# Kernel tuning notes

Measured on AMD Instinct MI355X. Metric: run time of the kernel, lower is better.

## Reference

```python
import jax, jax.numpy as jnp
import numpy as np

N_NODES = 100000
N_EDGES = 3200000
IN_DIM = 64
N_SEQ = 8
HID1 = 256
HID2 = 128
END = 64
OUT = 1


def _glorot(key, shape):
    fan_in, fan_out = shape
    lim = (6.0 / (fan_in + fan_out)) ** 0.5
    return jax.random.uniform(key, shape, jnp.float32, -lim, lim)


def setup_inputs() -> dict:
    key = jax.random.key(0)
    ks = jax.random.split(key, 10)
    features = jax.random.normal(ks[0], (N_NODES, IN_DIM, N_SEQ), jnp.float32)
    src = jax.random.randint(ks[1], (N_EDGES,), 0, N_NODES, jnp.int32)
    dst = jax.random.randint(ks[2], (N_EDGES,), 0, N_NODES, jnp.int32)
    return {
        "features": features,
        "src": src,
        "dst": dst,
        "W1": _glorot(ks[3], (IN_DIM * N_SEQ, HID1)),
        "b1": jnp.zeros((HID1,), jnp.float32),
        "W2": _glorot(ks[4], (HID1, HID2)),
        "b2": jnp.zeros((HID2,), jnp.float32),
        "Wo1": _glorot(ks[5], (HID2, END)),
        "bo1": jnp.zeros((END,), jnp.float32),
        "Wo2": _glorot(ks[6], (END, OUT)),
        "bo2": jnp.zeros((OUT,), jnp.float32),
    }


def _graph_conv(x, src, dst, W, b):
    # DGL GraphConv, norm='both': D_out^{-1/2} pre-scale, sum-aggregate, D_in^{-1/2} post-scale.
    n = x.shape[0]
    ones = jnp.ones((src.shape[0],), x.dtype)
    deg_out = jnp.clip(jax.ops.segment_sum(ones, src, num_segments=n), 1.0)
    deg_in = jnp.clip(jax.ops.segment_sum(ones, dst, num_segments=n), 1.0)
    x = x * jax.lax.rsqrt(deg_out)[:, None]
    # mult-first vs aggregate-first is mathematically identical; project to smaller dim first
    if W.shape[0] > W.shape[1]:
        x = x @ W
        agg = jax.ops.segment_sum(x[src], dst, num_segments=n)
    else:
        agg = jax.ops.segment_sum(x[src], dst, num_segments=n) @ W
    return agg * jax.lax.rsqrt(deg_in)[:, None] + b


def reference(features, src, dst, W1, b1, W2, b2, Wo1, bo1, Wo2, bo2):
    x = features.reshape(features.shape[0], IN_DIM * N_SEQ)  # [N, in_dim*n_seq]
    x = jax.nn.relu(_graph_conv(x, src, dst, W1, b1))
    x = _graph_conv(x, src, dst, W2, b2)
    x = jax.nn.relu(x @ Wo1 + bo1)
    return x @ Wo2 + bo2
```

## Files before the change

### kernel.cpp

```cpp
#include <hip/hip_runtime.h>
#include <hip/hip_bf16.h>
#include <hip/hip_fp16.h>

#define N_NODES 100000
#define N_EDGES 3200000
#define DIM0 512
#define DIM1 256
#define DIM2 128
#define DIM3 64
#define NSB 98

typedef _Float16 f16x8 __attribute__((ext_vector_type(8)));
typedef float f32x4 __attribute__((ext_vector_type(4)));


__global__ __launch_bounds__(256) void k_hist(const int* __restrict__ src,
                                              const int* __restrict__ dst,
                                              int* __restrict__ cnt_out,
                                              int* __restrict__ cnt_in,
                                              int* __restrict__ pos) {
    int e = blockIdx.x * 256 + threadIdx.x;
    if (e < N_EDGES) {
        atomicAdd(&cnt_out[src[e]], 1);
        pos[e] = atomicAdd(&cnt_in[dst[e]], 1);
    }
}

__global__ __launch_bounds__(1024) void k_scan_a(const int* __restrict__ cnt,
                                                 int* __restrict__ excl,
                                                 int* __restrict__ bsum) {
    __shared__ int buf[1024];
    int tid = threadIdx.x;
    int i = blockIdx.x * 1024 + tid;
    int v = (i < N_NODES) ? cnt[i] : 0;
    buf[tid] = v;
    __syncthreads();
    #pragma unroll
    for (int off = 1; off < 1024; off <<= 1) {
        int t = (tid >= off) ? buf[tid - off] : 0;
        __syncthreads();
        buf[tid] += t;
        __syncthreads();
    }
    if (i < N_NODES) excl[i] = buf[tid] - v;
    if (tid == 1023) bsum[blockIdx.x] = buf[1023];
}

__global__ __launch_bounds__(128) void k_scan_b(const int* __restrict__ bsum,
                                                int* __restrict__ boff) {
    __shared__ int buf[128];
    int tid = threadIdx.x;
    int v = (tid < NSB) ? bsum[tid] : 0;
    buf[tid] = v;
    __syncthreads();
    #pragma unroll
    for (int off = 1; off < 128; off <<= 1) {
        int t = (tid >= off) ? buf[tid - off] : 0;
        __syncthreads();
        buf[tid] += t;
        __syncthreads();
    }
    if (tid < NSB) boff[tid] = buf[tid] - v;
    if (tid == 127) boff[NSB] = buf[127];
}

__global__ __launch_bounds__(256) void k_scan_c(const int* __restrict__ excl,
                                                const int* __restrict__ boff,
                                                int* __restrict__ row_ptr) {
    int i = blockIdx.x * 256 + threadIdx.x;
    if (i < N_NODES) row_ptr[i] = excl[i] + boff[i >> 10];
    if (i == 0) row_ptr[N_NODES] = boff[NSB];
}

__global__ __launch_bounds__(256) void k_scatter(const int* __restrict__ src,
                                                 const int* __restrict__ dst,
                                                 const int* __restrict__ row_ptr,
                                                 const int* __restrict__ pos,
                                                 int* __restrict__ esrc) {
    int e = blockIdx.x * 256 + threadIdx.x;
    if (e < N_EDGES) esrc[row_ptr[dst[e]] + pos[e]] = src[e];
}

__global__ __launch_bounds__(256) void k_scales(const int* __restrict__ cnt_out,
                                                const int* __restrict__ cnt_in,
                                                float* __restrict__ s_out,
                                                float* __restrict__ s_in) {
    int i = blockIdx.x * 256 + threadIdx.x;
    if (i < N_NODES) {
        int co = cnt_out[i]; if (co < 1) co = 1;
        int ci = cnt_in[i];  if (ci < 1) ci = 1;
        s_out[i] = rsqrtf((float)co);
        s_in[i]  = rsqrtf((float)ci);
    }
}


__global__ __launch_bounds__(256) void k_cvtW1(const float* __restrict__ W1,
                                               __half* __restrict__ W1t) {
    int idx = blockIdx.x * 256 + threadIdx.x;
    if (idx < DIM0 * DIM1) {
        int k = idx / DIM1, n = idx % DIM1;
        W1t[n * DIM0 + k] = __float2half(W1[idx]);
    }
}

__global__ __launch_bounds__(256) void k_cvtW2(const float* __restrict__ W2,
                                               __half* __restrict__ W2t) {
    int idx = blockIdx.x * 256 + threadIdx.x;
    if (idx < DIM1 * DIM2) {
        int k = idx / DIM2, n = idx % DIM2;
        W2t[n * DIM1 + k] = __float2half(W2[idx]);
    }
}


__global__ __launch_bounds__(256) void k_gemm1(const float* __restrict__ feat,
                                               const float* __restrict__ s_out,
                                               const __half* __restrict__ W1t,
                                               __half* __restrict__ y) {
    __shared__ __align__(16) _Float16 As[64][40];
    __shared__ __align__(16) _Float16 Bs[256][40];
    int tid = threadIdx.x;
    int wv = tid >> 6, lane = tid & 63;
    int m16 = lane & 15, quad = lane >> 4;
    int n0 = blockIdx.x * 64;

    int srow = tid >> 2;
    int scol = (tid & 3) * 8;
    int gr = n0 + srow;
    bool avalid = gr < N_NODES;
    int grc = avalid ? gr : (N_NODES - 1);
    float ascale = avalid ? s_out[gr] : 0.0f;
    const float* aptr = feat + (size_t)grc * DIM0 + scol;
    int bn = tid >> 2;
    int bc = (tid & 3) * 8;

    f32x4 acc[4][4] = {};
    for (int k0 = 0; k0 < DIM0; k0 += 32) {
        float4 f0 = *(const float4*)(aptr + k0);
        float4 f1 = *(const float4*)(aptr + k0 + 4);
        __syncthreads();
        {
            f16x8 h;
            h[0] = (_Float16)(f0.x * ascale); h[1] = (_Float16)(f0.y * ascale);
            h[2] = (_Float16)(f0.z * ascale); h[3] = (_Float16)(f0.w * ascale);
            h[4] = (_Float16)(f1.x * ascale); h[5] = (_Float16)(f1.y * ascale);
            h[6] = (_Float16)(f1.z * ascale); h[7] = (_Float16)(f1.w * ascale);
            *(f16x8*)&As[srow][scol] = h;
        }
        #pragma unroll
        for (int p = 0; p < 4; ++p) {
            int n = p * 64 + bn;
            f16x8 v = *(const f16x8*)(W1t + (size_t)n * DIM0 + k0 + bc);
            *(f16x8*)&Bs[n][bc] = v;
        }
        __syncthreads();
        f16x8 af[4], bf[4];
        #pragma unroll
        for (int r = 0; r < 4; ++r) af[r] = *(const f16x8*)&As[r * 16 + m16][quad * 8];
        #pragma unroll
        for (int c = 0; c < 4; ++c) bf[c] = *(const f16x8*)&Bs[wv * 64 + c * 16 + m16][quad * 8];
        #pragma unroll
        for (int r = 0; r < 4; ++r)
            #pragma unroll
            for (int c = 0; c < 4; ++c)
                acc[r][c] = __builtin_amdgcn_mfma_f32_16x16x32_f16(af[r], bf[c], acc[r][c], 0, 0, 0);
    }
    #pragma unroll
    for (int r = 0; r < 4; ++r) {
        #pragma unroll
        for (int i = 0; i < 4; ++i) {
            int row = n0 + r * 16 + quad * 4 + i;
            if (row < N_NODES) {
                #pragma unroll
                for (int c = 0; c < 4; ++c) {
                    int col = wv * 64 + c * 16 + m16;
                    y[(size_t)row * DIM1 + col] = __float2half(acc[r][c][i]);
                }
            }
        }
    }
}


__global__ __launch_bounds__(256) void k_agg256(const int* __restrict__ row_ptr,
                                                const int* __restrict__ esrc,
                                                const __half* __restrict__ y1,
                                                const float* __restrict__ s_in,
                                                const float* __restrict__ s_out,
                                                const float* __restrict__ b1,
                                                __half* __restrict__ x2) {
    int wave = threadIdx.x >> 6;
    int lane = threadIdx.x & 63;
    int n = blockIdx.x * 4 + wave;
    int beg = row_ptr[n], end = row_ptr[n + 1];
    const uint2* ybase = (const uint2*)y1;
    float4 acc = make_float4(0.f, 0.f, 0.f, 0.f);
    int i = beg;
    for (; i + 4 <= end; i += 4) {
        int s0 = esrc[i], s1 = esrc[i + 1], s2 = esrc[i + 2], s3 = esrc[i + 3];
        uint2 r0 = ybase[(size_t)s0 * 64 + lane];
        uint2 r1 = ybase[(size_t)s1 * 64 + lane];
        uint2 r2 = ybase[(size_t)s2 * 64 + lane];
        uint2 r3 = ybase[(size_t)s3 * 64 + lane];
        float2 a0 = __half22float2(*(__half2*)&r0.x), b0 = __half22float2(*(__half2*)&r0.y);
        float2 a1 = __half22float2(*(__half2*)&r1.x), b1v = __half22float2(*(__half2*)&r1.y);
        float2 a2 = __half22float2(*(__half2*)&r2.x), b2v = __half22float2(*(__half2*)&r2.y);
        float2 a3 = __half22float2(*(__half2*)&r3.x), b3v = __half22float2(*(__half2*)&r3.y);
        acc.x += a0.x + a1.x + a2.x + a3.x;
        acc.y += a0.y + a1.y + a2.y + a3.y;
        acc.z += b0.x + b1v.x + b2v.x + b3v.x;
        acc.w += b0.y + b1v.y + b2v.y + b3v.y;
    }
    for (; i < end; ++i) {
        uint2 r = ybase[(size_t)esrc[i] * 64 + lane];
        float2 a = __half22float2(*(__half2*)&r.x), b = __half22float2(*(__half2*)&r.y);
        acc.x += a.x; acc.y += a.y; acc.z += b.x; acc.w += b.y;
    }
    float si = s_in[n];
    float so = s_out[n];
    float4 bb = *(const float4*)&b1[lane * 4];
    acc.x = fmaxf(acc.x * si + bb.x, 0.f) * so;
    acc.y = fmaxf(acc.y * si + bb.y, 0.f) * so;
    acc.z = fmaxf(acc.z * si + bb.z, 0.f) * so;
    acc.w = fmaxf(acc.w * si + bb.w, 0.f) * so;
    union { uint2 u; __half2 h[2]; } cv;
    cv.h[0] = __floats2half2_rn(acc.x, acc.y);
    cv.h[1] = __floats2half2_rn(acc.z, acc.w);
    *(uint2*)&x2[(size_t)n * DIM1 + lane * 4] = cv.u;
}


__global__ __launch_bounds__(256) void k_gemm2(const __half* __restrict__ x2,
                                               const __half* __restrict__ W2t,
                                               __half* __restrict__ y) {
    __shared__ __align__(16) _Float16 As[64][40];
    __shared__ __align__(16) _Float16 Bs[128][40];
    int tid = threadIdx.x;
    int wv = tid >> 6, lane = tid & 63;
    int m16 = lane & 15, quad = lane >> 4;
    int n0 = blockIdx.x * 64;

    int srow = tid >> 2;
    int scol = (tid & 3) * 8;
    int gr = n0 + srow;
    int grc = (gr < N_NODES) ? gr : (N_NODES - 1);
    const __half* aptr = x2 + (size_t)grc * DIM1 + scol;
    int bn = tid >> 2;
    int bc = (tid & 3) * 8;

    f32x4 acc[4][2] = {};
    for (int k0 = 0; k0 < DIM1; k0 += 32) {
        f16x8 av = *(const f16x8*)(aptr + k0);
        __syncthreads();
        *(f16x8*)&As[srow][scol] = av;
        #pragma unroll
        for (int p = 0; p < 2; ++p) {
            int n = p * 64 + bn;
            f16x8 v = *(const f16x8*)(W2t + (size_t)n * DIM1 + k0 + bc);
            *(f16x8*)&Bs[n][bc] = v;
        }
        __syncthreads();
        f16x8 af[4], bf[2];
        #pragma unroll
        for (int r = 0; r < 4; ++r) af[r] = *(const f16x8*)&As[r * 16 + m16][quad * 8];
        #pragma unroll
        for (int c = 0; c < 2; ++c) bf[c] = *(const f16x8*)&Bs[wv * 32 + c * 16 + m16][quad * 8];
        #pragma unroll
        for (int r = 0; r < 4; ++r)
            #pragma unroll
            for (int c = 0; c < 2; ++c)
                acc[r][c] = __builtin_amdgcn_mfma_f32_16x16x32_f16(af[r], bf[c], acc[r][c], 0, 0, 0);
    }
    #pragma unroll
    for (int r = 0; r < 4; ++r) {
        #pragma unroll
        for (int i = 0; i < 4; ++i) {
            int row = n0 + r * 16 + quad * 4 + i;
            if (row < N_NODES) {
                #pragma unroll
                for (int c = 0; c < 2; ++c) {
                    int col = wv * 32 + c * 16 + m16;
                    y[(size_t)row * DIM2 + col] = __float2half(acc[r][c][i]);
                }
            }
        }
    }
}


__global__ __launch_bounds__(256) void k_agg_head(const int* __restrict__ row_ptr,
                                                  const int* __restrict__ esrc,
                                                  const __half* __restrict__ y2,
                                                  const float* __restrict__ s_in,
                                                  const float* __restrict__ b2,
                                                  const float* __restrict__ Wo1,
                                                  const float* __restrict__ bo1,
                                                  const float* __restrict__ Wo2,
                                                  const float* __restrict__ bo2,
                                                  float* __restrict__ out) {
    __shared__ float w1s[DIM2 * DIM3];
    __shared__ float w2s[DIM3];
    __shared__ float hs[4][DIM2];
    int tid = threadIdx.x;
    for (int i = tid; i < DIM2 * DIM3; i += 256) w1s[i] = Wo1[i];
    if (tid < DIM3) w2s[tid] = Wo2[tid];
    __syncthreads();

    int wave = tid >> 6, lane = tid & 63;
    int n = blockIdx.x * 4 + wave;
    int beg = row_ptr[n], end = row_ptr[n + 1];
    const unsigned* ybase = (const unsigned*)y2;
    float2 acc = make_float2(0.f, 0.f);
    int i = beg;
    for (; i + 4 <= end; i += 4) {
        unsigned r0 = ybase[(size_t)esrc[i] * 64 + lane];
        unsigned r1 = ybase[(size_t)esrc[i + 1] * 64 + lane];
        unsigned r2 = ybase[(size_t)esrc[i + 2] * 64 + lane];
        unsigned r3 = ybase[(size_t)esrc[i + 3] * 64 + lane];
        float2 f0 = __half22float2(*(__half2*)&r0);
        float2 f1 = __half22float2(*(__half2*)&r1);
        float2 f2 = __half22float2(*(__half2*)&r2);
        float2 f3 = __half22float2(*(__half2*)&r3);
        acc.x += f0.x + f1.x + f2.x + f3.x;
        acc.y += f0.y + f1.y + f2.y + f3.y;
    }
    for (; i < end; ++i) {
        unsigned r = ybase[(size_t)esrc[i] * 64 + lane];
        float2 f = __half22float2(*(__half2*)&r);
        acc.x += f.x; acc.y += f.y;
    }
    float si = s_in[n];
    float2 bv = *(const float2*)&b2[lane * 2];
    hs[wave][lane * 2 + 0] = acc.x * si + bv.x;
    hs[wave][lane * 2 + 1] = acc.y * si + bv.y;
    __syncthreads();

    float t = bo1[lane];
    #pragma unroll 8
    for (int k = 0; k < DIM2; ++k) t += hs[wave][k] * w1s[k * DIM3 + lane];
    t = fmaxf(t, 0.f);
    float p = t * w2s[lane];
    #pragma unroll
    for (int off = 32; off > 0; off >>= 1) p += __shfl_down(p, off);
    if (lane == 0) out[n] = p + bo2[0];
}


extern "C" void kernel_launch(void* const* d_in, const int* in_sizes, int n_in,
                              void* d_out, int out_size, void* d_ws, size_t ws_size,
                              hipStream_t stream) {
    const float* feat = (const float*)d_in[0];
    const int*   src  = (const int*)d_in[1];
    const int*   dst  = (const int*)d_in[2];
    const float* W1   = (const float*)d_in[3];
    const float* b1   = (const float*)d_in[4];
    const float* W2   = (const float*)d_in[5];
    const float* b2   = (const float*)d_in[6];
    const float* Wo1  = (const float*)d_in[7];
    const float* bo1  = (const float*)d_in[8];
    const float* Wo2  = (const float*)d_in[9];
    const float* bo2  = (const float*)d_in[10];
    float* out = (float*)d_out;

    char* ws = (char*)d_ws;
    size_t off = 0;
    auto alloc = [&](size_t bytes) -> char* {
        char* p = ws + off;
        off = (off + bytes + 255) & ~(size_t)255;
        return p;
    };
    int*    cnt_out = (int*)alloc(N_NODES * 4);
    int*    cnt_in  = (int*)alloc(N_NODES * 4);
    int*    row_ptr = (int*)alloc((N_NODES + 1) * 4);
    int*    excl    = (int*)alloc(N_NODES * 4);
    int*    bsum    = (int*)alloc((NSB + 1) * 4);
    int*    boff    = (int*)alloc((NSB + 1) * 4);
    int*    pos     = (int*)alloc((size_t)N_EDGES * 4);
    int*    esrc    = (int*)alloc((size_t)N_EDGES * 4);
    float*  s_out   = (float*)alloc(N_NODES * 4);
    float*  s_in    = (float*)alloc(N_NODES * 4);
    __half* W1t     = (__half*)alloc((size_t)DIM0 * DIM1 * 2);
    __half* W2t     = (__half*)alloc((size_t)DIM1 * DIM2 * 2);
    __half* y1h     = (__half*)alloc((size_t)N_NODES * DIM1 * 2);
    __half* x2h     = (__half*)alloc((size_t)N_NODES * DIM1 * 2);
    __half* y2h     = (__half*)alloc((size_t)N_NODES * DIM2 * 2);

    hipMemsetAsync(cnt_out, 0, N_NODES * 4, stream);
    hipMemsetAsync(cnt_in, 0, N_NODES * 4, stream);

    k_hist<<<(N_EDGES + 255) / 256, 256, 0, stream>>>(src, dst, cnt_out, cnt_in, pos);
    k_scan_a<<<NSB, 1024, 0, stream>>>(cnt_in, excl, bsum);
    k_scan_b<<<1, 128, 0, stream>>>(bsum, boff);
    k_scan_c<<<(N_NODES + 255) / 256, 256, 0, stream>>>(excl, boff, row_ptr);
    k_scatter<<<(N_EDGES + 255) / 256, 256, 0, stream>>>(src, dst, row_ptr, pos, esrc);
    k_scales<<<(N_NODES + 255) / 256, 256, 0, stream>>>(cnt_out, cnt_in, s_out, s_in);

    k_cvtW1<<<(DIM0 * DIM1 + 255) / 256, 256, 0, stream>>>(W1, W1t);
    k_cvtW2<<<(DIM1 * DIM2 + 255) / 256, 256, 0, stream>>>(W2, W2t);

    int nblk = (N_NODES + 63) / 64;
    k_gemm1<<<nblk, 256, 0, stream>>>(feat, s_out, W1t, y1h);
    k_agg256<<<N_NODES / 4, 256, 0, stream>>>(row_ptr, esrc, y1h, s_in, s_out, b1, x2h);
    k_gemm2<<<nblk, 256, 0, stream>>>(x2h, W2t, y2h);
    k_agg_head<<<N_NODES / 4, 256, 0, stream>>>(row_ptr, esrc, y2h, s_in, b2,
                                                Wo1, bo1, Wo2, bo2, out);
}
```

Measured before the change: 1.172 ms.

## Build CSR degree histograms in LDS partitions and scatter via atomic cursors

Degree counting moves from per-edge global atomics to a partitioned shared-memory histogram: each block handles a 16K-node slice and flushes nonzero bins to global. Because the per-edge position array no longer exists, the scatter step claims slots with an atomic cursor per destination, and the scales kernel is fused into the scan finalisation. The goal is to cut global atomic traffic and the 12.8MB pos write and read. In exchange, each block re-reads the full edge arrays (14 partition passes), and edge order within a row becomes nondeterministic, which can change floating-point summation order.

```diff
diff --git a/kernel.cpp b/kernel.cpp
--- a/kernel.cpp
+++ b/kernel.cpp
@@ -10,19 +10,38 @@
 #define DIM3 64
 #define NSB 98
 
+#define HPART 16384
+#define NPARTS 7
+#define HBLK 32
+
 typedef _Float16 f16x8 __attribute__((ext_vector_type(8)));
 typedef float f32x4 __attribute__((ext_vector_type(4)));
 
 
-__global__ __launch_bounds__(256) void k_hist(const int* __restrict__ src,
-                                              const int* __restrict__ dst,
-                                              int* __restrict__ cnt_out,
-                                              int* __restrict__ cnt_in,
-                                              int* __restrict__ pos) {
-    int e = blockIdx.x * 256 + threadIdx.x;
-    if (e < N_EDGES) {
-        atomicAdd(&cnt_out[src[e]], 1);
-        pos[e] = atomicAdd(&cnt_in[dst[e]], 1);
+__global__ __launch_bounds__(256) void k_hist_lds(const int* __restrict__ src,
+                                                  const int* __restrict__ dst,
+                                                  int* __restrict__ cnt_out,
+                                                  int* __restrict__ cnt_in) {
+    __shared__ int h[HPART];
+    int job = blockIdx.x / HBLK;
+    int sub = blockIdx.x % HBLK;
+    int arr = job / NPARTS;
+    int part = job % NPARTS;
+    int base = part * HPART;
+    const int* __restrict__ keys = arr ? dst : src;
+    int* __restrict__ cnt = arr ? cnt_in : cnt_out;
+
+    for (int i = threadIdx.x; i < HPART; i += 256) h[i] = 0;
+    __syncthreads();
+    for (int e = sub * 256 + threadIdx.x; e < N_EDGES; e += HBLK * 256) {
+        int k = keys[e] - base;
+        if ((unsigned)k < (unsigned)HPART) atomicAdd(&h[k], 1);
+    }
+    __syncthreads();
+    int lim = N_NODES - base; if (lim > HPART) lim = HPART;
+    for (int i = threadIdx.x; i < lim; i += 256) {
+        int v = h[i];
+        if (v) atomicAdd(&cnt[base + i], v);
     }
 }
 
@@ -66,31 +85,33 @@
 
 __global__ __launch_bounds__(256) void k_scan_c(const int* __restrict__ excl,
                                                 const int* __restrict__ boff,
-                                                int* __restrict__ row_ptr) {
-    int i = blockIdx.x * 256 + threadIdx.x;
-    if (i < N_NODES) row_ptr[i] = excl[i] + boff[i >> 10];
-    if (i == 0) row_ptr[N_NODES] = boff[NSB];
-}
-
-__global__ __launch_bounds__(256) void k_scatter(const int* __restrict__ src,
-                                                 const int* __restrict__ dst,
-                                                 const int* __restrict__ row_ptr,
-                                                 const int* __restrict__ pos,
-                                                 int* __restrict__ esrc) {
-    int e = blockIdx.x * 256 + threadIdx.x;
-    if (e < N_EDGES) esrc[row_ptr[dst[e]] + pos[e]] = src[e];
-}
-
-__global__ __launch_bounds__(256) void k_scales(const int* __restrict__ cnt_out,
+                                                const int* __restrict__ cnt_out,
                                                 const int* __restrict__ cnt_in,
+                                                int* __restrict__ row_ptr,
+                                                int* __restrict__ cursor,
                                                 float* __restrict__ s_out,
                                                 float* __restrict__ s_in) {
     int i = blockIdx.x * 256 + threadIdx.x;
     if (i < N_NODES) {
+        int rp = excl[i] + boff[i >> 10];
+        row_ptr[i] = rp;
+        cursor[i] = rp;
         int co = cnt_out[i]; if (co < 1) co = 1;
         int ci = cnt_in[i];  if (ci < 1) ci = 1;
         s_out[i] = rsqrtf((float)co);
         s_in[i]  = rsqrtf((float)ci);
+    }
+    if (i == 0) row_ptr[N_NODES] = boff[NSB];
+}
+
+__global__ __launch_bounds__(256) void k_scatter(const int* __restrict__ src,
+                                                 const int* __restrict__ dst,
+                                                 int* __restrict__ cursor,
+                                                 int* __restrict__ esrc) {
+    int e = blockIdx.x * 256 + threadIdx.x;
+    if (e < N_EDGES) {
+        int p = atomicAdd(&cursor[dst[e]], 1);
+        esrc[p] = src[e];
     }
 }
 
@@ -373,10 +394,10 @@
     int*    cnt_out = (int*)alloc(N_NODES * 4);
     int*    cnt_in  = (int*)alloc(N_NODES * 4);
     int*    row_ptr = (int*)alloc((N_NODES + 1) * 4);
+    int*    cursor  = (int*)alloc(N_NODES * 4);
     int*    excl    = (int*)alloc(N_NODES * 4);
     int*    bsum    = (int*)alloc((NSB + 1) * 4);
     int*    boff    = (int*)alloc((NSB + 1) * 4);
-    int*    pos     = (int*)alloc((size_t)N_EDGES * 4);
     int*    esrc    = (int*)alloc((size_t)N_EDGES * 4);
     float*  s_out   = (float*)alloc(N_NODES * 4);
     float*  s_in    = (float*)alloc(N_NODES * 4);
@@ -389,12 +410,12 @@
     hipMemsetAsync(cnt_out, 0, N_NODES * 4, stream);
     hipMemsetAsync(cnt_in, 0, N_NODES * 4, stream);
 
-    k_hist<<<(N_EDGES + 255) / 256, 256, 0, stream>>>(src, dst, cnt_out, cnt_in, pos);
+    k_hist_lds<<<2 * NPARTS * HBLK, 256, 0, stream>>>(src, dst, cnt_out, cnt_in);
     k_scan_a<<<NSB, 1024, 0, stream>>>(cnt_in, excl, bsum);
     k_scan_b<<<1, 128, 0, stream>>>(bsum, boff);
-    k_scan_c<<<(N_NODES + 255) / 256, 256, 0, stream>>>(excl, boff, row_ptr);
-    k_scatter<<<(N_EDGES + 255) / 256, 256, 0, stream>>>(src, dst, row_ptr, pos, esrc);
-    k_scales<<<(N_NODES + 255) / 256, 256, 0, stream>>>(cnt_out, cnt_in, s_out, s_in);
+    k_scan_c<<<(N_NODES + 255) / 256, 256, 0, stream>>>(excl, boff, cnt_out, cnt_in,
+                                                        row_ptr, cursor, s_out, s_in);
+    k_scatter<<<(N_EDGES + 255) / 256, 256, 0, stream>>>(src, dst, cursor, esrc);
 
     k_cvtW1<<<(DIM0 * DIM1 + 255) / 256, 256, 0, stream>>>(W1, W1t);
     k_cvtW2<<<(DIM1 * DIM2 + 255) / 256, 256, 0, stream>>>(W2, W2t);
```

Result: slower. 1.283 ms (+9.5%).
